# Kernel tuning notes

Hardware: AMD Instinct MI355X
Metric: run time of the kernel (lower is better)

Reference implementation:

```python
import jax, jax.numpy as jnp
import numpy as np

N = 50000
E = 800000
IN_DIM = 64
HID = 64
OUT = 40


def setup_inputs() -> dict:
    key = jax.random.key(0)
    ks = jax.random.split(key, 10)
    x = jax.random.normal(ks[0], (N, IN_DIM), dtype=jnp.float32)
    edge_index = jax.random.randint(ks[1], (2, E), 0, N, dtype=jnp.int64)

    def lin(k, fan_in, fan_out):
        # torch nn.Linear default init: U(-1/sqrt(fan_in), 1/sqrt(fan_in))
        bound = 1.0 / np.sqrt(fan_in)
        kw, kb = jax.random.split(k)
        W = jax.random.uniform(kw, (fan_in, fan_out), minval=-bound, maxval=bound, dtype=jnp.float32)
        b = jax.random.uniform(kb, (fan_out,), minval=-bound, maxval=bound, dtype=jnp.float32)
        return W, b

    W1, b1 = lin(ks[2], IN_DIM, HID)   # conv layer 1
    W2, b2 = lin(ks[3], HID, HID)      # conv layer 2
    Wp1, bp1 = lin(ks[4], HID, HID)    # post_mp linear 1
    Wp2, bp2 = lin(ks[5], HID, OUT)    # post_mp linear 2
    return {"x": x, "edge_index": edge_index,
            "W1": W1, "b1": b1, "W2": W2, "b2": b2,
            "Wp1": Wp1, "bp1": bp1, "Wp2": Wp2, "bp2": bp2}


def _mean_aggregate(h, src, dst, num_nodes):
    # Row-normalized sparse adjacency matmul: out[i] = (1/deg(i)) * sum_{(i,j) in E} h[j]
    # adj[src, dst] = 1/deg(src), where deg(src) = #outgoing edges of src.
    ones = jnp.ones((src.shape[0],), dtype=h.dtype)
    deg = jax.ops.segment_sum(ones, src, num_segments=num_nodes)
    w = 1.0 / deg[src]                         # [E], every src has deg >= 1
    msgs = h[dst] * w[:, None]                 # [E, d] gather + scale
    return jax.ops.segment_sum(msgs, src, num_segments=num_nodes)  # [N, d]


def reference(x, edge_index, W1, b1, W2, b2, Wp1, bp1, Wp2, bp2):
    src = edge_index[0]
    dst = edge_index[1]
    n = x.shape[0]
    # GraphSAGEConvolution layer 1: (dropout=eval noop) linear -> spmm mean-agg -> relu
    h = x @ W1 + b1
    h = _mean_aggregate(h, src, dst, n)
    h = jax.nn.relu(h)
    # GraphSAGEConvolution layer 2
    h = h @ W2 + b2
    h = _mean_aggregate(h, src, dst, n)
    h = jax.nn.relu(h)
    # post_mp: Linear -> (dropout noop) -> Linear
    h = h @ Wp1 + bp1
    h = h @ Wp2 + bp2
    return jax.nn.log_softmax(h, axis=1)
```

## Files before the change

### kernel.cpp

```cpp
#include <hip/hip_runtime.h>
#include <cmath>


typedef _Float16 half_t;
typedef half_t half2_t __attribute__((ext_vector_type(2)));

#if defined(__has_builtin)
# if __has_builtin(__builtin_amdgcn_fdot2)
#  define FDOT2(a, b, c) __builtin_amdgcn_fdot2((a), (b), (c), false)
# endif
#endif
#ifndef FDOT2
# define FDOT2(a, b, c) fmaf((float)(a)[0], (float)(b)[0], fmaf((float)(a)[1], (float)(b)[1], (c)))
#endif

#define NXCD 8
#define CAP  64
#define EDGE_BLOCKS 1024
#define WS 66

__global__ __launch_bounds__(256) void build_h1(
    const int* __restrict__ src, const int* __restrict__ dst,
    const float* __restrict__ x, const float* __restrict__ W1,
    const float* __restrict__ b1,
    const float* __restrict__ W2, const float* __restrict__ Wp1,
    const float* __restrict__ Wp2,
    half_t* __restrict__ Wt, int* __restrict__ cnt,
    unsigned short* __restrict__ col, half_t* __restrict__ Hh,
    int E, int N)
{
    const int tid = threadIdx.x;

    if (blockIdx.x < EDGE_BLOCKS) {
        int gid = blockIdx.x * 256 + tid;
        if (gid < 3 * 4096) {
            int which = gid >> 12, r = gid & 4095;
            int c = r >> 6, k = r & 63;
            float v;
            if      (which == 0) v = W2[k * 64 + c];
            else if (which == 1) v = Wp1[k * 64 + c];
            else                 v = (c < 40) ? Wp2[k * 40 + c] : 0.f;
            Wt[gid] = (half_t)v;
        }

        const int g     = blockIdx.x & (NXCD - 1);
        const int bpg   = blockIdx.x >> 3;
        const int nbpg  = EDGE_BLOCKS >> 3;
        const int chunk = (N + NXCD - 1) / NXCD;
        const int lo = g * chunk;
        const int hi = min(N, lo + chunk);
        const int4* src4 = (const int4*)src;
        const int quads = E >> 2;
        for (int q = bpg * 256 + tid; q < quads; q += nbpg * 256) {
            int4 s4 = src4[q];
            int e = q * 4;
            if (s4.x >= lo && s4.x < hi) {
                int pos = atomicAdd(&cnt[s4.x], 1);
                if (pos < CAP) col[(size_t)s4.x * CAP + pos] = (unsigned short)dst[e + 0];
            }
            if (s4.y >= lo && s4.y < hi) {
                int pos = atomicAdd(&cnt[s4.y], 1);
                if (pos < CAP) col[(size_t)s4.y * CAP + pos] = (unsigned short)dst[e + 1];
            }
            if (s4.z >= lo && s4.z < hi) {
                int pos = atomicAdd(&cnt[s4.z], 1);
                if (pos < CAP) col[(size_t)s4.z * CAP + pos] = (unsigned short)dst[e + 2];
            }
            if (s4.w >= lo && s4.w < hi) {
                int pos = atomicAdd(&cnt[s4.w], 1);
                if (pos < CAP) col[(size_t)s4.w * CAP + pos] = (unsigned short)dst[e + 3];
            }
        }
        if (blockIdx.x == 0 && tid < (E & 3)) {
            int e = (E & ~3) + tid;
            int s = src[e];
            int pos = atomicAdd(&cnt[s], 1);
            if (pos < CAP) col[(size_t)s * CAP + pos] = (unsigned short)dst[e];
        }
    } else {
        __shared__ half_t xs[16][64];
        const int lane = tid & 63;
        const int wid  = tid >> 6;
        const int row0 = (blockIdx.x - EDGE_BLOCKS) * 16;

        for (int i = tid; i < 16 * 64; i += 256) {
            int rr = row0 + (i >> 6);
            float v = (rr < N) ? x[(size_t)row0 * 64 + i] : 0.f;
            xs[i >> 6][i & 63] = (half_t)v;
        }
        const float bias = b1[lane];
        __syncthreads();

        float acc[4] = {bias, bias, bias, bias};
#pragma unroll 1
        for (int c = 0; c < 4; ++c) {
            half2_t wr[8];
#pragma unroll
            for (int j = 0; j < 8; ++j) {
                float a0 = W1[(c * 16 + 2 * j + 0) * 64 + lane];
                float a1 = W1[(c * 16 + 2 * j + 1) * 64 + lane];
                half2_t h; h[0] = (half_t)a0; h[1] = (half_t)a1;
                wr[j] = h;
            }
#pragma unroll
            for (int r = 0; r < 4; ++r) {
                const half2_t* xp = (const half2_t*)&xs[wid * 4 + r][c * 16];
#pragma unroll
                for (int j = 0; j < 8; ++j) acc[r] = FDOT2(xp[j], wr[j], acc[r]);
            }
        }
#pragma unroll
        for (int r = 0; r < 4; ++r) {
            int grow = row0 + wid * 4 + r;
            if (grow < N) Hh[(size_t)grow * 64 + lane] = (half_t)acc[r];
        }
    }
}

__device__ __forceinline__ void gather_node(const half2_t* __restrict__ H2,
                                            const unsigned short* __restrict__ cbase,
                                            int deg, int hf, int sub,
                                            float& ax, float& ay) {
    ax = 0.f; ay = 0.f;
    int e = 0;
    for (; e + 16 <= deg; e += 16) {
        int t0 = cbase[e +  0 + hf], t1 = cbase[e +  2 + hf];
        int t2 = cbase[e +  4 + hf], t3 = cbase[e +  6 + hf];
        int t4 = cbase[e +  8 + hf], t5 = cbase[e + 10 + hf];
        int t6 = cbase[e + 12 + hf], t7 = cbase[e + 14 + hf];
        half2_t f0 = H2[(size_t)t0 * 32 + sub];
        half2_t f1 = H2[(size_t)t1 * 32 + sub];
        half2_t f2 = H2[(size_t)t2 * 32 + sub];
        half2_t f3 = H2[(size_t)t3 * 32 + sub];
        half2_t f4 = H2[(size_t)t4 * 32 + sub];
        half2_t f5 = H2[(size_t)t5 * 32 + sub];
        half2_t f6 = H2[(size_t)t6 * 32 + sub];
        half2_t f7 = H2[(size_t)t7 * 32 + sub];
        ax += (((float)f0[0] + (float)f1[0]) + ((float)f2[0] + (float)f3[0]))
            + (((float)f4[0] + (float)f5[0]) + ((float)f6[0] + (float)f7[0]));
        ay += (((float)f0[1] + (float)f1[1]) + ((float)f2[1] + (float)f3[1]))
            + (((float)f4[1] + (float)f5[1]) + ((float)f6[1] + (float)f7[1]));
    }
    for (; e + 2 <= deg; e += 2) {
        half2_t f = H2[(size_t)cbase[e + hf] * 32 + sub];
        ax += (float)f[0]; ay += (float)f[1];
    }
    if (e < deg && hf == 0) {
        half2_t f = H2[(size_t)cbase[e] * 32 + sub];
        ax += (float)f[0]; ay += (float)f[1];
    }
    ax += __shfl_xor(ax, 32);
    ay += __shfl_xor(ay, 32);
}

__device__ __forceinline__ void stage_w(const half_t* __restrict__ Wt,
                                        half_t* __restrict__ wlds, int tid, int nthr) {
    const unsigned* ws = (const unsigned*)Wt;
    unsigned* wd = (unsigned*)wlds;
    for (int i = tid; i < 2048; i += nthr) {
        int c = i >> 5, kp = i & 31;
        wd[c * (WS / 2) + kp] = ws[i];
    }
}

__global__ __launch_bounds__(1024) void fused_gather_gemm(
    const half_t* __restrict__ H, const int* __restrict__ cnt,
    const unsigned short* __restrict__ colb, const half_t* __restrict__ Wt,
    const float* __restrict__ b, half_t* __restrict__ Y, int N)
{
    __shared__ half_t wlds[64 * WS];
    __shared__ half_t xrow[16][64];
    const int tid  = threadIdx.x;
    const int w    = tid >> 6;
    const int lane = tid & 63;
    const int hf   = lane >> 5;
    const int sub  = lane & 31;

    stage_w(Wt, wlds, tid, 1024);
    __syncthreads();

    const int node = blockIdx.x * 16 + w;
    if (node >= N) return;

    const int deg = cnt[node];
    float ax, ay;
    gather_node((const half2_t*)H, colb + (size_t)node * CAP, deg, hf, sub, ax, ay);
    if (hf == 0) {
        float inv = (deg > 0) ? 1.f / (float)deg : 0.f;
        half2_t o;
        o[0] = (half_t)fmaxf(ax * inv, 0.f);
        o[1] = (half_t)fmaxf(ay * inv, 0.f);
        ((half2_t*)xrow[w])[sub] = o;
    }

    float acc = b[lane];
    const half2_t* wl = (const half2_t*)(wlds + (size_t)lane * WS);
    const half2_t* xp = (const half2_t*)xrow[w];
#pragma unroll
    for (int i = 0; i < 32; ++i) acc = FDOT2(xp[i], wl[i], acc);
    Y[(size_t)node * 64 + lane] = (half_t)acc;
}

__global__ __launch_bounds__(1024) void fused_gather_post(
    const half_t* __restrict__ H, const int* __restrict__ cnt,
    const unsigned short* __restrict__ colb,
    const half_t* __restrict__ Wt1, const float* __restrict__ bp1,
    const half_t* __restrict__ Wt2, const float* __restrict__ bp2,
    float* __restrict__ out, int N)
{
    __shared__ half_t w1lds[64 * WS];
    __shared__ half_t w2lds[64 * WS];
    __shared__ half_t xrow[16][64];
    __shared__ half_t yrow[16][64];
    const int tid  = threadIdx.x;
    const int w    = tid >> 6;
    const int lane = tid & 63;
    const int hf   = lane >> 5;
    const int sub  = lane & 31;

    stage_w(Wt1, w1lds, tid, 1024);
    stage_w(Wt2, w2lds, tid, 1024);
    __syncthreads();

    const int node = blockIdx.x * 16 + w;
    if (node >= N) return;

    const int deg = cnt[node];
    float ax, ay;
    gather_node((const half2_t*)H, colb + (size_t)node * CAP, deg, hf, sub, ax, ay);
    if (hf == 0) {
        float inv = (deg > 0) ? 1.f / (float)deg : 0.f;
        half2_t o;
        o[0] = (half_t)fmaxf(ax * inv, 0.f);
        o[1] = (half_t)fmaxf(ay * inv, 0.f);
        ((half2_t*)xrow[w])[sub] = o;
    }

    {
        float acc = bp1[lane];
        const half2_t* wl = (const half2_t*)(w1lds + (size_t)lane * WS);
        const half2_t* xp = (const half2_t*)xrow[w];
#pragma unroll
        for (int i = 0; i < 32; ++i) acc = FDOT2(xp[i], wl[i], acc);
        yrow[w][lane] = (half_t)acc;
    }

    float acc = (lane < 40) ? bp2[lane] : 0.f;
    {
        const half2_t* wl = (const half2_t*)(w2lds + (size_t)lane * WS);
        const half2_t* yp = (const half2_t*)yrow[w];
#pragma unroll
        for (int i = 0; i < 32; ++i) acc = FDOT2(yp[i], wl[i], acc);
    }
    float vm = (lane < 40) ? acc : -INFINITY;
    float m = vm;
#pragma unroll
    for (int o = 32; o; o >>= 1) m = fmaxf(m, __shfl_xor(m, o));
    float e = (lane < 40) ? expf(vm - m) : 0.f;
    float s = e;
#pragma unroll
    for (int o = 32; o; o >>= 1) s += __shfl_xor(s, o);
    float ls = logf(s);
    if (lane < 40) out[(size_t)node * 40 + lane] = vm - m - ls;
}

extern "C" void kernel_launch(void* const* d_in, const int* in_sizes, int n_in,
                              void* d_out, int out_size, void* d_ws, size_t ws_size,
                              hipStream_t stream) {
    const float* x   = (const float*)d_in[0];
    const int*   ei  = (const int*)d_in[1];
    const float* W1  = (const float*)d_in[2];
    const float* b1  = (const float*)d_in[3];
    const float* W2  = (const float*)d_in[4];
    const float* b2  = (const float*)d_in[5];
    const float* Wp1 = (const float*)d_in[6];
    const float* bp1 = (const float*)d_in[7];
    const float* Wp2 = (const float*)d_in[8];
    const float* bp2 = (const float*)d_in[9];
    float* out = (float*)d_out;

    const int N = in_sizes[0] / 64;
    const int E = in_sizes[1] / 2;
    const int* src = ei;
    const int* dst = ei + E;

    char*  wsb = (char*)d_ws;
    size_t off = 0;
    auto alloc = [&](size_t bytes) { void* p = wsb + off; off += (bytes + 511) & ~(size_t)511; return p; };
    int*            cnt = (int*)alloc((size_t)N * 4);
    unsigned short* col = (unsigned short*)alloc((size_t)N * CAP * 2);
    half_t*         Wt  = (half_t*)alloc((size_t)3 * 4096 * 2);
    half_t*         Ha  = (half_t*)alloc((size_t)N * 64 * 2);
    half_t*         Hb  = (half_t*)alloc((size_t)N * 64 * 2);
    (void)ws_size; (void)n_in; (void)out_size;

    const int nb16 = (N + 15) / 16;

    hipMemsetAsync(cnt, 0, (size_t)N * 4, stream);
    build_h1<<<EDGE_BLOCKS + nb16, 256, 0, stream>>>(src, dst, x, W1, b1, W2, Wp1, Wp2,
                                                     Wt, cnt, col, Ha, E, N);
    fused_gather_gemm<<<nb16, 1024, 0, stream>>>(Ha, cnt, col, Wt + 0 * 4096, b2, Hb, N);
    fused_gather_post<<<nb16, 1024, 0, stream>>>(Hb, cnt, col, Wt + 1 * 4096, bp1,
                                                 Wt + 2 * 4096, bp2, out, N);
}
```

Baseline: 151.9 us.

## Shuffle-broadcast neighbor indices, accumulate in fp16, and shrink gather blocks to 512 threads

Each wave now loads a node's 64 neighbor indices in one coalesced read and broadcasts them with __shfl, replacing repeated scalar index loads. The 16-edge inner loop accumulates in packed fp16 before converting to float. The two gather kernels now launch 512-thread blocks handling 8 nodes each, and the small GEMVs use two accumulators for more ILP. The fp16 accumulation can lose precision, and the smaller blocks stage the LDS weights twice as often in total.

```diff
diff --git a/kernel.cpp b/kernel.cpp
--- a/kernel.cpp
+++ b/kernel.cpp
@@ -119,35 +119,32 @@
 
 __device__ __forceinline__ void gather_node(const half2_t* __restrict__ H2,
                                             const unsigned short* __restrict__ cbase,
-                                            int deg, int hf, int sub,
+                                            int deg, int hf, int sub, int lane,
                                             float& ax, float& ay) {
     ax = 0.f; ay = 0.f;
+    const int myt = (int)cbase[lane];
     int e = 0;
     for (; e + 16 <= deg; e += 16) {
-        int t0 = cbase[e +  0 + hf], t1 = cbase[e +  2 + hf];
-        int t2 = cbase[e +  4 + hf], t3 = cbase[e +  6 + hf];
-        int t4 = cbase[e +  8 + hf], t5 = cbase[e + 10 + hf];
-        int t6 = cbase[e + 12 + hf], t7 = cbase[e + 14 + hf];
-        half2_t f0 = H2[(size_t)t0 * 32 + sub];
-        half2_t f1 = H2[(size_t)t1 * 32 + sub];
-        half2_t f2 = H2[(size_t)t2 * 32 + sub];
-        half2_t f3 = H2[(size_t)t3 * 32 + sub];
-        half2_t f4 = H2[(size_t)t4 * 32 + sub];
-        half2_t f5 = H2[(size_t)t5 * 32 + sub];
-        half2_t f6 = H2[(size_t)t6 * 32 + sub];
-        half2_t f7 = H2[(size_t)t7 * 32 + sub];
-        ax += (((float)f0[0] + (float)f1[0]) + ((float)f2[0] + (float)f3[0]))
-            + (((float)f4[0] + (float)f5[0]) + ((float)f6[0] + (float)f7[0]));
-        ay += (((float)f0[1] + (float)f1[1]) + ((float)f2[1] + (float)f3[1]))
-            + (((float)f4[1] + (float)f5[1]) + ((float)f6[1] + (float)f7[1]));
+        half2_t hacc; hacc[0] = (half_t)0.f; hacc[1] = (half_t)0.f;
+#pragma unroll
+        for (int i = 0; i < 8; ++i) {
+            int t = __shfl(myt, e + 2 * i + hf);
+            hacc += H2[(size_t)t * 32 + sub];
+        }
+        ax += (float)hacc[0];
+        ay += (float)hacc[1];
     }
     for (; e + 2 <= deg; e += 2) {
-        half2_t f = H2[(size_t)cbase[e + hf] * 32 + sub];
+        int t = __shfl(myt, e + hf);
+        half2_t f = H2[(size_t)t * 32 + sub];
         ax += (float)f[0]; ay += (float)f[1];
     }
-    if (e < deg && hf == 0) {
-        half2_t f = H2[(size_t)cbase[e] * 32 + sub];
-        ax += (float)f[0]; ay += (float)f[1];
+    if (e < deg) {
+        int t = __shfl(myt, e);
+        if (hf == 0) {
+            half2_t f = H2[(size_t)t * 32 + sub];
+            ax += (float)f[0]; ay += (float)f[1];
+        }
     }
     ax += __shfl_xor(ax, 32);
     ay += __shfl_xor(ay, 32);
@@ -163,28 +160,28 @@
     }
 }
 
-__global__ __launch_bounds__(1024) void fused_gather_gemm(
+__global__ __launch_bounds__(512) void fused_gather_gemm(
     const half_t* __restrict__ H, const int* __restrict__ cnt,
     const unsigned short* __restrict__ colb, const half_t* __restrict__ Wt,
     const float* __restrict__ b, half_t* __restrict__ Y, int N)
 {
     __shared__ half_t wlds[64 * WS];
-    __shared__ half_t xrow[16][64];
+    __shared__ half_t xrow[8][64];
     const int tid  = threadIdx.x;
     const int w    = tid >> 6;
     const int lane = tid & 63;
     const int hf   = lane >> 5;
     const int sub  = lane & 31;
 
-    stage_w(Wt, wlds, tid, 1024);
+    stage_w(Wt, wlds, tid, 512);
     __syncthreads();
 
-    const int node = blockIdx.x * 16 + w;
+    const int node = blockIdx.x * 8 + w;
     if (node >= N) return;
 
     const int deg = cnt[node];
     float ax, ay;
-    gather_node((const half2_t*)H, colb + (size_t)node * CAP, deg, hf, sub, ax, ay);
+    gather_node((const half2_t*)H, colb + (size_t)node * CAP, deg, hf, sub, lane, ax, ay);
     if (hf == 0) {
         float inv = (deg > 0) ? 1.f / (float)deg : 0.f;
         half2_t o;
@@ -193,15 +190,18 @@
         ((half2_t*)xrow[w])[sub] = o;
     }
 
-    float acc = b[lane];
+    float a0 = b[lane], a1 = 0.f;
     const half2_t* wl = (const half2_t*)(wlds + (size_t)lane * WS);
     const half2_t* xp = (const half2_t*)xrow[w];
 #pragma unroll
-    for (int i = 0; i < 32; ++i) acc = FDOT2(xp[i], wl[i], acc);
-    Y[(size_t)node * 64 + lane] = (half_t)acc;
-}
-
-__global__ __launch_bounds__(1024) void fused_gather_post(
+    for (int i = 0; i < 16; ++i) {
+        a0 = FDOT2(xp[2 * i + 0], wl[2 * i + 0], a0);
+        a1 = FDOT2(xp[2 * i + 1], wl[2 * i + 1], a1);
+    }
+    Y[(size_t)node * 64 + lane] = (half_t)(a0 + a1);
+}
+
+__global__ __launch_bounds__(512) void fused_gather_post(
     const half_t* __restrict__ H, const int* __restrict__ cnt,
     const unsigned short* __restrict__ colb,
     const half_t* __restrict__ Wt1, const float* __restrict__ bp1,
@@ -210,24 +210,24 @@
 {
     __shared__ half_t w1lds[64 * WS];
     __shared__ half_t w2lds[64 * WS];
-    __shared__ half_t xrow[16][64];
-    __shared__ half_t yrow[16][64];
+    __shared__ half_t xrow[8][64];
+    __shared__ half_t yrow[8][64];
     const int tid  = threadIdx.x;
     const int w    = tid >> 6;
     const int lane = tid & 63;
     const int hf   = lane >> 5;
     const int sub  = lane & 31;
 
-    stage_w(Wt1, w1lds, tid, 1024);
-    stage_w(Wt2, w2lds, tid, 1024);
+    stage_w(Wt1, w1lds, tid, 512);
+    stage_w(Wt2, w2lds, tid, 512);
     __syncthreads();
 
-    const int node = blockIdx.x * 16 + w;
+    const int node = blockIdx.x * 8 + w;
     if (node >= N) return;
 
     const int deg = cnt[node];
     float ax, ay;
-    gather_node((const half2_t*)H, colb + (size_t)node * CAP, deg, hf, sub, ax, ay);
+    gather_node((const half2_t*)H, colb + (size_t)node * CAP, deg, hf, sub, lane, ax, ay);
     if (hf == 0) {
         float inv = (deg > 0) ? 1.f / (float)deg : 0.f;
         half2_t o;
@@ -237,21 +237,28 @@
     }
 
     {
-        float acc = bp1[lane];
+        float a0 = bp1[lane], a1 = 0.f;
         const half2_t* wl = (const half2_t*)(w1lds + (size_t)lane * WS);
         const half2_t* xp = (const half2_t*)xrow[w];
 #pragma unroll
-        for (int i = 0; i < 32; ++i) acc = FDOT2(xp[i], wl[i], acc);
-        yrow[w][lane] = (half_t)acc;
-    }
-
-    float acc = (lane < 40) ? bp2[lane] : 0.f;
+        for (int i = 0; i < 16; ++i) {
+            a0 = FDOT2(xp[2 * i + 0], wl[2 * i + 0], a0);
+            a1 = FDOT2(xp[2 * i + 1], wl[2 * i + 1], a1);
+        }
+        yrow[w][lane] = (half_t)(a0 + a1);
+    }
+
+    float a0 = (lane < 40) ? bp2[lane] : 0.f, a1 = 0.f;
     {
         const half2_t* wl = (const half2_t*)(w2lds + (size_t)lane * WS);
         const half2_t* yp = (const half2_t*)yrow[w];
 #pragma unroll
-        for (int i = 0; i < 32; ++i) acc = FDOT2(yp[i], wl[i], acc);
-    }
+        for (int i = 0; i < 16; ++i) {
+            a0 = FDOT2(yp[2 * i + 0], wl[2 * i + 0], a0);
+            a1 = FDOT2(yp[2 * i + 1], wl[2 * i + 1], a1);
+        }
+    }
+    float acc = a0 + a1;
     float vm = (lane < 40) ? acc : -INFINITY;
     float m = vm;
 #pragma unroll
@@ -295,11 +302,12 @@
     (void)ws_size; (void)n_in; (void)out_size;
 
     const int nb16 = (N + 15) / 16;
+    const int nb8  = (N + 7) / 8;
 
     hipMemsetAsync(cnt, 0, (size_t)N * 4, stream);
     build_h1<<<EDGE_BLOCKS + nb16, 256, 0, stream>>>(src, dst, x, W1, b1, W2, Wp1, Wp2,
                                                      Wt, cnt, col, Ha, E, N);
-    fused_gather_gemm<<<nb16, 1024, 0, stream>>>(Ha, cnt, col, Wt + 0 * 4096, b2, Hb, N);
-    fused_gather_post<<<nb16, 1024, 0, stream>>>(Hb, cnt, col, Wt + 1 * 4096, bp1,
-                                                 Wt + 2 * 4096, bp2, out, N);
-}
+    fused_gather_gemm<<<nb8, 512, 0, stream>>>(Ha, cnt, col, Wt + 0 * 4096, b2, Hb, N);
+    fused_gather_post<<<nb8, 512, 0, stream>>>(Hb, cnt, col, Wt + 1 * 4096, bp1,
+                                               Wt + 2 * 4096, bp2, out, N);
+}
```

Result: faster. 138.5 us (-8.8%).
